# Performance work log

Measured on AMD Instinct MI355X. Metric: run time of the kernel, lower is better.

## Reference

```python
import jax, jax.numpy as jnp
import numpy as np

K_MAX, K_MIN = 12.0, 1.0
TEMP = 1.0
STE_ALPHA = 12.0
EPS = 1e-8

DIM, HID, KHID, WHID = 512, 2048, 128, 128
B, N = 8, 1024


def setup_inputs() -> dict:
    key = jax.random.key(0)
    ks = jax.random.split(key, 13)
    def lin(k, fan_in, shape):
        bound = 1.0 / np.sqrt(fan_in)
        return jax.random.uniform(k, shape, jnp.float32, -bound, bound)
    return {
        "x": jax.random.normal(ks[0], (B, N, DIM), jnp.float32),
        "fc1_w": lin(ks[1], DIM, (HID, DIM)),
        "fc1_b": lin(ks[2], DIM, (HID,)),
        "fc2_w": lin(ks[3], HID, (DIM, HID)),
        "fc2_b": lin(ks[4], HID, (DIM,)),
        "k1_w": lin(ks[5], DIM, (KHID, DIM)),
        "k1_b": lin(ks[6], DIM, (KHID,)),
        "k2_w": lin(ks[7], KHID, (3, KHID)),
        "k2_b": lin(ks[8], KHID, (3,)),
        "w1_w": lin(ks[9], DIM, (WHID, DIM)),
        "w1_b": lin(ks[10], DIM, (WHID,)),
        "w2_w": lin(ks[11], WHID, (3, WHID)),
        "w2_b": lin(ks[12], WHID, (3,)),
    }


def adaptive_knn_aggregate(h, k_cont):
    # h: (B,N,C), k_cont: (B,) continuous k in [k_min, k_max]
    sim = jnp.einsum("bnc,bmc->bnm", h, h) / TEMP          # (B,N,N)
    order = jnp.argsort(-sim, axis=-1)                      # descending
    rank = jnp.argsort(order, axis=-1).astype(h.dtype)      # rank 0 = most similar
    # soft top-k gate (STE-style sigmoid around k_cont)
    gate = jax.nn.sigmoid(STE_ALPHA * (k_cont[:, None, None] - (rank + 0.5)))
    attn = jax.nn.softmax(sim, axis=-1) * gate
    attn = attn / (attn.sum(axis=-1, keepdims=True) + EPS)
    return jnp.einsum("bnm,bmc->bnc", attn, h)


def reference(x, fc1_w, fc1_b, fc2_w, fc2_b, k1_w, k1_b, k2_w, k2_b,
              w1_w, w1_b, w2_w, w2_b):
    pooled = x.mean(axis=1)                                 # (B,C)
    # adaptive k values net
    kh = jax.nn.relu(pooled @ k1_w.T + k1_b)
    ratio = jax.nn.sigmoid(kh @ k2_w.T + k2_b)              # (B,3)
    k_cont = K_MIN + ratio * (K_MAX - K_MIN)
    # adaptive branch weights net
    wh = jax.nn.relu(pooled @ w1_w.T + w1_b)
    w = jax.nn.softmax(wh @ w2_w.T + w2_b, axis=-1)         # (B,3)
    # MLP (dropout p=0 -> identity)
    h = jax.nn.relu(x @ fc1_w.T + fc1_b)
    h = h @ fc2_w.T + fc2_b                                 # (B,N,C)
    # three KNN aggregation branches blended by w
    y = sum(adaptive_knn_aggregate(h, k_cont[:, i]) * w[:, i, None, None]
            for i in range(3))
    return y
```

## Files before the change

### kernel.cpp

```cpp
#include <hip/hip_runtime.h>
#include <math.h>

#define DIM_ 512
#define HID_ 2048
#define B_ 8
#define N_ 1024
#define ROWS_ 8192
#define TOPK 16

typedef __attribute__((ext_vector_type(8))) short short8;
typedef __attribute__((ext_vector_type(4))) float float4v;

__device__ __forceinline__ float sigm(float x) { return 1.f / (1.f + __expf(-x)); }

__device__ __forceinline__ short f2bf(float f) {
    unsigned u = __float_as_uint(f);
    u += 0x7FFF + ((u >> 16) & 1);
    return (short)(u >> 16);
}

__device__ __forceinline__ float bf2f(unsigned short s) {
    return __uint_as_float((unsigned)s << 16);
}

__device__ __forceinline__ unsigned f2ord(float f) {
    unsigned u = __float_as_uint(f);
    return (u & 0x80000000u) ? ~u : (u | 0x80000000u);
}
__device__ __forceinline__ float ord2f(unsigned o) {
    unsigned u = (o & 0x80000000u) ? (o & 0x7FFFFFFFu) : ~o;
    return __uint_as_float(u);
}

__device__ __forceinline__ void gload16(const short* g, short* l) {
    __builtin_amdgcn_global_load_lds(
        (const __attribute__((address_space(1))) void*)g,
        (__attribute__((address_space(3))) void*)l, 16, 0, 0);
}

__global__ __launch_bounds__(256)
void cvt_bf16_kernel(const float* __restrict__ in, short* __restrict__ out, int n4) {
    const int i = blockIdx.x * 256 + threadIdx.x;
    if (i < n4) {
        const float4 v = *(const float4*)(in + (long long)i * 4);
        short4 o;
        o.x = f2bf(v.x); o.y = f2bf(v.y); o.z = f2bf(v.z); o.w = f2bf(v.w);
        *(short4*)(out + (long long)i * 4) = o;
    }
}

__global__ __launch_bounds__(512)
void pool_part_kernel(const float* __restrict__ x, float* __restrict__ part) {
    const int bx = blockIdx.x;
    const int b = bx >> 5, chunk = bx & 31;
    const int c = threadIdx.x;
    const float* xb = x + ((long long)b * N_ + chunk * 32) * DIM_ + c;
    float s = 0.f;
    for (int n = 0; n < 32; ++n) s += xb[(long long)n * DIM_];
    part[(long long)bx * DIM_ + c] = s;
}

__global__ __launch_bounds__(512)
void pool_reduce_kernel(const float* __restrict__ part, float* __restrict__ pooled) {
    const int b = blockIdx.x;
    const int c = threadIdx.x;
    float s = 0.f;
    for (int g = 0; g < 32; ++g) s += part[((long long)b * 32 + g) * DIM_ + c];
    pooled[b * DIM_ + c] = s * (1.f / 1024.f);
}

__global__ __launch_bounds__(128)
void heads_kernel(const float* __restrict__ pooled,
                  const float* __restrict__ k1w, const float* __restrict__ k1b,
                  const float* __restrict__ k2w, const float* __restrict__ k2b,
                  const float* __restrict__ w1w, const float* __restrict__ w1b,
                  const float* __restrict__ w2w, const float* __restrict__ w2b,
                  float* __restrict__ kcont, float* __restrict__ wbr) {
    const int b = blockIdx.x;
    const int t = threadIdx.x;
    __shared__ float sp[DIM_];
    __shared__ float kh[128], wh[128];
    __shared__ float wraw[4];
    for (int i = t; i < DIM_; i += 128) sp[i] = pooled[b * DIM_ + i];
    __syncthreads();
    float ak = k1b[t], aw = w1b[t];
    for (int k = 0; k < DIM_; ++k) {
        float pv = sp[k];
        ak = fmaf(pv, k1w[t * DIM_ + k], ak);
        aw = fmaf(pv, w1w[t * DIM_ + k], aw);
    }
    kh[t] = fmaxf(ak, 0.f);
    wh[t] = fmaxf(aw, 0.f);
    __syncthreads();
    if (t < 3) {
        float rk = k2b[t], rw = w2b[t];
        for (int k = 0; k < 128; ++k) {
            rk = fmaf(kh[k], k2w[t * 128 + k], rk);
            rw = fmaf(wh[k], w2w[t * 128 + k], rw);
        }
        kcont[b * 3 + t] = 1.f + 11.f * sigm(rk);
        wraw[t] = rw;
    }
    __syncthreads();
    if (t == 0) {
        float m = fmaxf(wraw[0], fmaxf(wraw[1], wraw[2]));
        float e0 = __expf(wraw[0] - m), e1 = __expf(wraw[1] - m), e2 = __expf(wraw[2] - m);
        float inv = 1.f / (e0 + e1 + e2);
        wbr[b * 3 + 0] = e0 * inv;
        wbr[b * 3 + 1] = e1 * inv;
        wbr[b * 3 + 2] = e2 * inv;
    }
}

template<int OUTMODE>
__global__ __launch_bounds__(256)
void gemm_mfma(const short* __restrict__ A, const short* __restrict__ Bm,
               const float* __restrict__ bias,
               float* __restrict__ outF, short* __restrict__ outB,
               int M, int N, int K, int lda, int ldb,
               long long sA, long long sB, long long sC) {
    const int bz = blockIdx.z;
    A  += (long long)bz * sA;
    Bm += (long long)bz * sB;

    __shared__ short As[128 * 64];
    __shared__ short Bs[128 * 64];

    const int tid = threadIdx.x;
    const int lane = tid & 63;
    const int wv = tid >> 6;
    const int m0 = blockIdx.y * 128;
    const int n0 = blockIdx.x * 128;

    const int lrow = lane >> 3;
    const int cg = (lane & 7) ^ lrow;

    const int ml = (wv & 1) * 64;
    const int nl = (wv >> 1) * 64;
    const int fr = lane & 15;
    const int kq = lane >> 4;

    float4v acc[4][4];
#pragma unroll
    for (int i = 0; i < 4; ++i)
#pragma unroll
        for (int j = 0; j < 4; ++j) acc[i][j] = (float4v){0.f, 0.f, 0.f, 0.f};

    for (int k0 = 0; k0 < K; k0 += 64) {
        __syncthreads();
#pragma unroll
        for (int i = 0; i < 4; ++i) {
            const int rloc = wv * 32 + i * 8 + lrow;
            gload16(A + (long long)(m0 + rloc) * lda + (k0 + cg * 8),
                    &As[(wv * 32 + i * 8) * 64]);
            gload16(Bm + (long long)(n0 + rloc) * ldb + (k0 + cg * 8),
                    &Bs[(wv * 32 + i * 8) * 64]);
        }
        __syncthreads();
#pragma unroll
        for (int ks = 0; ks < 2; ++ks) {
            const int c = ks * 4 + kq;
            short8 af[4], bfr[4];
#pragma unroll
            for (int i = 0; i < 4; ++i) {
                const int m = ml + i * 16 + fr;
                af[i] = *(const short8*)&As[m * 64 + ((c ^ (m & 7)) * 8)];
                const int n = nl + i * 16 + fr;
                bfr[i] = *(const short8*)&Bs[n * 64 + ((c ^ (n & 7)) * 8)];
            }
#pragma unroll
            for (int i = 0; i < 4; ++i)
#pragma unroll
                for (int j = 0; j < 4; ++j)
                    acc[i][j] = __builtin_amdgcn_mfma_f32_16x16x32_bf16(
                        af[i], bfr[j], acc[i][j], 0, 0, 0);
        }
    }

    const long long outOfs = (long long)bz * sC;
#pragma unroll
    for (int i = 0; i < 4; ++i) {
#pragma unroll
        for (int j = 0; j < 4; ++j) {
            const int ng = n0 + nl + j * 16 + fr;
            float bv = 0.f;
            if (OUTMODE != 2) bv = bias[ng];
#pragma unroll
            for (int r = 0; r < 4; ++r) {
                const int mg = m0 + ml + i * 16 + kq * 4 + r;
                float v = acc[i][j][r] + bv;
                if (OUTMODE == 0) v = fmaxf(v, 0.f);
                const long long idx = outOfs + (long long)mg * N + ng;
                if (OUTMODE == 2) outF[idx] = v;
                else              outB[idx] = f2bf(v);
            }
        }
    }
}

__global__ __launch_bounds__(256)
void combine_kernel(const float* __restrict__ p0, const float* __restrict__ p1,
                    const float* __restrict__ bias, short* __restrict__ out) {
    const int i = blockIdx.x * 256 + threadIdx.x;
    const long long o = (long long)i * 4;
    const float4 a = *(const float4*)(p0 + o);
    const float4 b = *(const float4*)(p1 + o);
    const int col = (int)(o & (DIM_ - 1));
    const float4 bs = *(const float4*)(bias + col);
    short4 r;
    r.x = f2bf(a.x + b.x + bs.x);
    r.y = f2bf(a.y + b.y + bs.y);
    r.z = f2bf(a.z + b.z + bs.z);
    r.w = f2bf(a.w + b.w + bs.w);
    *(short4*)(out + o) = r;
}

__global__ __launch_bounds__(256)
void topk_kernel(const float* __restrict__ sim,
                 const float* __restrict__ kcont, const float* __restrict__ wbr,
                 int* __restrict__ gidx, float* __restrict__ gcoef) {
    const int wv = threadIdx.x >> 6;
    const int lane = threadIdx.x & 63;
    const int row = blockIdx.x * 4 + wv;
    const int b = row >> 10;
    const float* srow = sim + (long long)row * N_;

    float f[16];
    const int base = lane * 16;
#pragma unroll
    for (int q = 0; q < 4; ++q) {
        const float4 v = *(const float4*)(srow + base + q * 4);
        f[q * 4 + 0] = v.x; f[q * 4 + 1] = v.y; f[q * 4 + 2] = v.z; f[q * 4 + 3] = v.w;
    }

    float lmax = f[0];
#pragma unroll
    for (int j = 1; j < 16; ++j) lmax = fmaxf(lmax, f[j]);
#pragma unroll
    for (int d = 32; d > 0; d >>= 1) lmax = fmaxf(lmax, __shfl_xor(lmax, d));
    const float maxv = lmax;

    float lsum = 0.f;
#pragma unroll
    for (int j = 0; j < 16; ++j) lsum += __expf(f[j] - maxv);
#pragma unroll
    for (int d = 32; d > 0; d >>= 1) lsum += __shfl_xor(lsum, d);
    const float invden = 1.f / lsum;

    unsigned long long s[16];
#pragma unroll
    for (int j = 0; j < 16; ++j)
        s[j] = ((unsigned long long)f2ord(f[j]) << 32) | (unsigned)(1024 - (base + j));

    const float kc0 = kcont[b * 3 + 0], kc1 = kcont[b * 3 + 1], kc2 = kcont[b * 3 + 2];
    const float w0 = wbr[b * 3 + 0], w1 = wbr[b * 3 + 1], w2 = wbr[b * 3 + 2];

    float s0 = 0.f, s1 = 0.f, s2 = 0.f;
    float myp = 0.f;
    int myidx = 0;
    unsigned prevlo = 0xFFFFFFFFu;

#pragma unroll
    for (int r = 0; r < TOPK; ++r) {
        unsigned long long lm = 0;
#pragma unroll
        for (int j = 0; j < 16; ++j) {
            if ((unsigned)s[j] == prevlo) s[j] = 0;
            lm = (s[j] > lm) ? s[j] : lm;
        }
        unsigned long long gm = lm;
#pragma unroll
        for (int d = 32; d > 0; d >>= 1) {
            unsigned long long o = __shfl_xor(gm, d);
            gm = (o > gm) ? o : gm;
        }
        prevlo = (unsigned)gm;
        const float v = ord2f((unsigned)(gm >> 32));
        const int idx = 1024 - (int)(gm & 0xFFFFFFFFu);
        const float p = __expf(v - maxv) * invden;
        const float rr = (float)r + 0.5f;
        s0 += p * sigm(12.f * (kc0 - rr));
        s1 += p * sigm(12.f * (kc1 - rr));
        s2 += p * sigm(12.f * (kc2 - rr));
        if (lane == r) { myp = p; myidx = idx; }
    }

    const float f0 = w0 / (s0 + 1e-8f);
    const float f1 = w1 / (s1 + 1e-8f);
    const float f2 = w2 / (s2 + 1e-8f);
    if (lane < TOPK) {
        const float rr = (float)lane + 0.5f;
        const float coef = myp * (f0 * sigm(12.f * (kc0 - rr)) +
                                  f1 * sigm(12.f * (kc1 - rr)) +
                                  f2 * sigm(12.f * (kc2 - rr)));
        gidx[row * TOPK + lane] = myidx;
        gcoef[row * TOPK + lane] = coef;
    }
}

__global__ __launch_bounds__(128)
void aggregate_kernel(const unsigned short* __restrict__ h, const float* __restrict__ gcoef,
                      const int* __restrict__ gidx, float* __restrict__ y) {
    const int row = blockIdx.x;
    const int b = row >> 10;
    const unsigned short* hb = h + (long long)b * (N_ * DIM_);
    __shared__ float sc[TOPK];
    __shared__ int sidx[TOPK];
    const int tid = threadIdx.x;
    if (tid < TOPK) { sc[tid] = gcoef[row * TOPK + tid]; sidx[tid] = gidx[row * TOPK + tid]; }
    __syncthreads();
    const int c = tid << 2;
    float4 acc = make_float4(0.f, 0.f, 0.f, 0.f);
#pragma unroll
    for (int r = 0; r < TOPK; ++r) {
        const float wv = sc[r];
        const ushort4 hv = *(const ushort4*)(hb + (long long)sidx[r] * DIM_ + c);
        acc.x = fmaf(wv, bf2f(hv.x), acc.x);
        acc.y = fmaf(wv, bf2f(hv.y), acc.y);
        acc.z = fmaf(wv, bf2f(hv.z), acc.z);
        acc.w = fmaf(wv, bf2f(hv.w), acc.w);
    }
    *(float4*)(y + (long long)row * DIM_ + c) = acc;
}

extern "C" void kernel_launch(void* const* d_in, const int* in_sizes, int n_in,
                              void* d_out, int out_size, void* d_ws, size_t ws_size,
                              hipStream_t stream) {
    const float* x     = (const float*)d_in[0];
    const float* fc1_w = (const float*)d_in[1];
    const float* fc1_b = (const float*)d_in[2];
    const float* fc2_w = (const float*)d_in[3];
    const float* fc2_b = (const float*)d_in[4];
    const float* k1_w  = (const float*)d_in[5];
    const float* k1_b  = (const float*)d_in[6];
    const float* k2_w  = (const float*)d_in[7];
    const float* k2_b  = (const float*)d_in[8];
    const float* w1_w  = (const float*)d_in[9];
    const float* w1_b  = (const float*)d_in[10];
    const float* w2_w  = (const float*)d_in[11];
    const float* w2_b  = (const float*)d_in[12];

    char* ws = (char*)d_ws;
    short* h1b    = (short*)(ws + 0);
    float* simbuf = (float*)(ws + 0);
    short* xb     = (short*)(ws + 33554432);
    float* part0  = (float*)(ws + 33554432);
    float* part1  = (float*)(ws + 50331648);
    short* hb     = (short*)(ws + 67108864);
    short* w1b    = (short*)(ws + 75497472);
    short* w2b    = (short*)(ws + 77594624);
    float* ppart  = (float*)(ws + 79691776);
    float* pooled = (float*)(ws + 80216064);
    float* kcont  = (float*)(ws + 80232448);
    float* wbr    = (float*)(ws + 80232576);
    int*   topki  = (int*)  (ws + 80232704);
    float* topkc  = (float*)(ws + 80756992);

    float* y = (float*)d_out;

    cvt_bf16_kernel<<<dim3(ROWS_ * DIM_ / 4 / 256), dim3(256), 0, stream>>>(x, xb, ROWS_ * DIM_ / 4);
    cvt_bf16_kernel<<<dim3(HID_ * DIM_ / 4 / 256), dim3(256), 0, stream>>>(fc1_w, w1b, HID_ * DIM_ / 4);
    cvt_bf16_kernel<<<dim3(DIM_ * HID_ / 4 / 256), dim3(256), 0, stream>>>(fc2_w, w2b, DIM_ * HID_ / 4);

    pool_part_kernel<<<dim3(B_ * 32), dim3(512), 0, stream>>>(x, ppart);
    pool_reduce_kernel<<<dim3(B_), dim3(512), 0, stream>>>(ppart, pooled);
    heads_kernel<<<dim3(B_), dim3(128), 0, stream>>>(pooled, k1_w, k1_b, k2_w, k2_b,
                                                     w1_w, w1_b, w2_w, w2_b, kcont, wbr);

    gemm_mfma<0><<<dim3(HID_ / 128, ROWS_ / 128, 1), dim3(256), 0, stream>>>(
        xb, w1b, fc1_b, nullptr, h1b, ROWS_, HID_, DIM_, DIM_, DIM_, 0, 0, 0);
    gemm_mfma<2><<<dim3(DIM_ / 128, ROWS_ / 128, 2), dim3(256), 0, stream>>>(
        h1b, w2b, nullptr, part0, nullptr, ROWS_, DIM_, HID_ / 2, HID_, HID_,
        (long long)(HID_ / 2), (long long)(HID_ / 2), (long long)ROWS_ * DIM_);
    combine_kernel<<<dim3(ROWS_ * DIM_ / 4 / 256), dim3(256), 0, stream>>>(part0, part1, fc2_b, hb);
    gemm_mfma<2><<<dim3(N_ / 128, N_ / 128, B_), dim3(256), 0, stream>>>(
        hb, hb, nullptr, simbuf, nullptr, N_, N_, DIM_, DIM_, DIM_,
        (long long)N_ * DIM_, (long long)N_ * DIM_, (long long)N_ * N_);

    topk_kernel<<<dim3(ROWS_ / 4), dim3(256), 0, stream>>>(simbuf, kcont, wbr, topki, topkc);
    aggregate_kernel<<<dim3(ROWS_), dim3(128), 0, stream>>>(
        (const unsigned short*)hb, topkc, topki, y);
}
```

Baseline: 259.5 us.

## Fuse top-k selection with aggregation and use bitonic sort-merge selection

Replaces the 16-round iterative wave-wide argmax with a per-lane bitonic sort of 16 keys, then a butterfly merge across lanes so every lane ends up holding the global top 16. The aggregation is folded into the same kernel: each lane gathers 8 bf16 columns of h for each selected neighbor and writes y directly. This removes the intermediate index and coefficient buffers and one kernel launch. In exchange it uses many more registers for the 64-bit keys and shuffle buffers, which could lower occupancy.

```diff
diff --git a/kernel.cpp b/kernel.cpp
--- a/kernel.cpp
+++ b/kernel.cpp
@@ -216,9 +216,9 @@
 }
 
 __global__ __launch_bounds__(256)
-void topk_kernel(const float* __restrict__ sim,
-                 const float* __restrict__ kcont, const float* __restrict__ wbr,
-                 int* __restrict__ gidx, float* __restrict__ gcoef) {
+void topk_agg_kernel(const float* __restrict__ sim,
+                     const float* __restrict__ kcont, const float* __restrict__ wbr,
+                     const unsigned short* __restrict__ h, float* __restrict__ y) {
     const int wv = threadIdx.x >> 6;
     const int lane = threadIdx.x & 63;
     const int row = blockIdx.x * 4 + wv;
@@ -247,80 +247,93 @@
     for (int d = 32; d > 0; d >>= 1) lsum += __shfl_xor(lsum, d);
     const float invden = 1.f / lsum;
 
-    unsigned long long s[16];
+    unsigned long long key[16];
 #pragma unroll
     for (int j = 0; j < 16; ++j)
-        s[j] = ((unsigned long long)f2ord(f[j]) << 32) | (unsigned)(1024 - (base + j));
+        key[j] = ((unsigned long long)f2ord(f[j]) << 32) | (unsigned)(1024 - (base + j));
+
+#pragma unroll
+    for (int k = 2; k <= 16; k <<= 1) {
+#pragma unroll
+        for (int j = k >> 1; j > 0; j >>= 1) {
+#pragma unroll
+            for (int i = 0; i < 16; ++i) {
+                const int l = i ^ j;
+                if (l > i) {
+                    const bool desc = ((i & k) == 0);
+                    const unsigned long long a = key[i], bk = key[l];
+                    const bool sw = desc ? (a < bk) : (a > bk);
+                    key[i] = sw ? bk : a;
+                    key[l] = sw ? a : bk;
+                }
+            }
+        }
+    }
+
+#pragma unroll
+    for (int d = 1; d < 64; d <<= 1) {
+        unsigned long long other[16];
+#pragma unroll
+        for (int i = 0; i < 16; ++i)
+            other[i] = __shfl_xor(key[15 - i], d);
+#pragma unroll
+        for (int i = 0; i < 16; ++i)
+            key[i] = (key[i] > other[i]) ? key[i] : other[i];
+#pragma unroll
+        for (int j = 8; j > 0; j >>= 1) {
+#pragma unroll
+            for (int i = 0; i < 16; ++i) {
+                if ((i & j) == 0) {
+                    const unsigned long long a = key[i], bk = key[i | j];
+                    const bool sw = (a < bk);
+                    key[i] = sw ? bk : a;
+                    key[i | j] = sw ? a : bk;
+                }
+            }
+        }
+    }
 
     const float kc0 = kcont[b * 3 + 0], kc1 = kcont[b * 3 + 1], kc2 = kcont[b * 3 + 2];
     const float w0 = wbr[b * 3 + 0], w1 = wbr[b * 3 + 1], w2 = wbr[b * 3 + 2];
 
+    float p[16], g0[16], g1[16], g2[16];
     float s0 = 0.f, s1 = 0.f, s2 = 0.f;
-    float myp = 0.f;
-    int myidx = 0;
-    unsigned prevlo = 0xFFFFFFFFu;
-
-#pragma unroll
-    for (int r = 0; r < TOPK; ++r) {
-        unsigned long long lm = 0;
-#pragma unroll
-        for (int j = 0; j < 16; ++j) {
-            if ((unsigned)s[j] == prevlo) s[j] = 0;
-            lm = (s[j] > lm) ? s[j] : lm;
-        }
-        unsigned long long gm = lm;
-#pragma unroll
-        for (int d = 32; d > 0; d >>= 1) {
-            unsigned long long o = __shfl_xor(gm, d);
-            gm = (o > gm) ? o : gm;
-        }
-        prevlo = (unsigned)gm;
-        const float v = ord2f((unsigned)(gm >> 32));
-        const int idx = 1024 - (int)(gm & 0xFFFFFFFFu);
-        const float p = __expf(v - maxv) * invden;
+#pragma unroll
+    for (int r = 0; r < 16; ++r) {
+        const float v = ord2f((unsigned)(key[r] >> 32));
+        p[r] = __expf(v - maxv) * invden;
         const float rr = (float)r + 0.5f;
-        s0 += p * sigm(12.f * (kc0 - rr));
-        s1 += p * sigm(12.f * (kc1 - rr));
-        s2 += p * sigm(12.f * (kc2 - rr));
-        if (lane == r) { myp = p; myidx = idx; }
-    }
-
+        g0[r] = sigm(12.f * (kc0 - rr));
+        g1[r] = sigm(12.f * (kc1 - rr));
+        g2[r] = sigm(12.f * (kc2 - rr));
+        s0 = fmaf(p[r], g0[r], s0);
+        s1 = fmaf(p[r], g1[r], s1);
+        s2 = fmaf(p[r], g2[r], s2);
+    }
     const float f0 = w0 / (s0 + 1e-8f);
     const float f1 = w1 / (s1 + 1e-8f);
     const float f2 = w2 / (s2 + 1e-8f);
-    if (lane < TOPK) {
-        const float rr = (float)lane + 0.5f;
-        const float coef = myp * (f0 * sigm(12.f * (kc0 - rr)) +
-                                  f1 * sigm(12.f * (kc1 - rr)) +
-                                  f2 * sigm(12.f * (kc2 - rr)));
-        gidx[row * TOPK + lane] = myidx;
-        gcoef[row * TOPK + lane] = coef;
-    }
-}
-
-__global__ __launch_bounds__(128)
-void aggregate_kernel(const unsigned short* __restrict__ h, const float* __restrict__ gcoef,
-                      const int* __restrict__ gidx, float* __restrict__ y) {
-    const int row = blockIdx.x;
-    const int b = row >> 10;
-    const unsigned short* hb = h + (long long)b * (N_ * DIM_);
-    __shared__ float sc[TOPK];
-    __shared__ int sidx[TOPK];
-    const int tid = threadIdx.x;
-    if (tid < TOPK) { sc[tid] = gcoef[row * TOPK + tid]; sidx[tid] = gidx[row * TOPK + tid]; }
-    __syncthreads();
-    const int c = tid << 2;
-    float4 acc = make_float4(0.f, 0.f, 0.f, 0.f);
-#pragma unroll
-    for (int r = 0; r < TOPK; ++r) {
-        const float wv = sc[r];
-        const ushort4 hv = *(const ushort4*)(hb + (long long)sidx[r] * DIM_ + c);
-        acc.x = fmaf(wv, bf2f(hv.x), acc.x);
-        acc.y = fmaf(wv, bf2f(hv.y), acc.y);
-        acc.z = fmaf(wv, bf2f(hv.z), acc.z);
-        acc.w = fmaf(wv, bf2f(hv.w), acc.w);
-    }
-    *(float4*)(y + (long long)row * DIM_ + c) = acc;
+
+    const unsigned short* hbase = h + (long long)b * (N_ * DIM_) + lane * 8;
+    float acc[8] = {0.f, 0.f, 0.f, 0.f, 0.f, 0.f, 0.f, 0.f};
+#pragma unroll
+    for (int r = 0; r < 16; ++r) {
+        const int idx = 1024 - (int)(key[r] & 0xFFFFFFFFu);
+        const float coef = p[r] * (f0 * g0[r] + f1 * g1[r] + f2 * g2[r]);
+        const ushort4 h0 = *(const ushort4*)(hbase + (long long)idx * DIM_);
+        const ushort4 h1 = *(const ushort4*)(hbase + (long long)idx * DIM_ + 4);
+        acc[0] = fmaf(coef, bf2f(h0.x), acc[0]);
+        acc[1] = fmaf(coef, bf2f(h0.y), acc[1]);
+        acc[2] = fmaf(coef, bf2f(h0.z), acc[2]);
+        acc[3] = fmaf(coef, bf2f(h0.w), acc[3]);
+        acc[4] = fmaf(coef, bf2f(h1.x), acc[4]);
+        acc[5] = fmaf(coef, bf2f(h1.y), acc[5]);
+        acc[6] = fmaf(coef, bf2f(h1.z), acc[6]);
+        acc[7] = fmaf(coef, bf2f(h1.w), acc[7]);
+    }
+    float* yp = y + (long long)row * DIM_ + lane * 8;
+    *(float4*)(yp + 0) = make_float4(acc[0], acc[1], acc[2], acc[3]);
+    *(float4*)(yp + 4) = make_float4(acc[4], acc[5], acc[6], acc[7]);
 }
 
 extern "C" void kernel_launch(void* const* d_in, const int* in_sizes, int n_in,
@@ -353,8 +366,6 @@
     float* pooled = (float*)(ws + 80216064);
     float* kcont  = (float*)(ws + 80232448);
     float* wbr    = (float*)(ws + 80232576);
-    int*   topki  = (int*)  (ws + 80232704);
-    float* topkc  = (float*)(ws + 80756992);
 
     float* y = (float*)d_out;
 
@@ -377,7 +388,6 @@
         hb, hb, nullptr, simbuf, nullptr, N_, N_, DIM_, DIM_, DIM_,
         (long long)N_ * DIM_, (long long)N_ * DIM_, (long long)N_ * N_);
 
-    topk_kernel<<<dim3(ROWS_ / 4), dim3(256), 0, stream>>>(simbuf, kcont, wbr, topki, topkc);
-    aggregate_kernel<<<dim3(ROWS_), dim3(128), 0, stream>>>(
-        (const unsigned short*)hb, topkc, topki, y);
-}
+    topk_agg_kernel<<<dim3(ROWS_ / 4), dim3(256), 0, stream>>>(
+        simbuf, kcont, wbr, (const unsigned short*)hb, y);
+}
```

New measurement: 261.3 us. Within noise of the previous version (+0.7%).
